# Performance work log

Measured on AMD Instinct MI355X. Metric: run time of the kernel, lower is better.

Reference implementation:

```python
import jax, jax.numpy as jnp
import numpy as np

B, N, D, R, H = 8192, 256, 6, 3, 32


def setup_inputs() -> dict:
    key = jax.random.key(0)
    ks = jax.random.split(key, 8)
    neighbor_states = jax.random.normal(ks[0], (B, N, D), dtype=jnp.float32)
    neighbor_roles = jax.random.randint(ks[1], (B, N), 0, R, dtype=jnp.int32)
    neighbor_mask = jax.random.randint(ks[2], (B, N), 0, 2, dtype=jnp.int32).astype(jnp.bool_)
    trust_weights = jax.random.uniform(ks[3], (B, N), dtype=jnp.float32)
    # per-role MLP params: Linear(D,H) -> ReLU -> Linear(H,1)
    s1 = 1.0 / np.sqrt(D)
    s2 = 1.0 / np.sqrt(H)
    W1 = jax.random.uniform(ks[4], (R, D, H), minval=-s1, maxval=s1, dtype=jnp.float32)
    b1 = jax.random.uniform(ks[5], (R, H), minval=-s1, maxval=s1, dtype=jnp.float32)
    W2 = jax.random.uniform(ks[6], (R, H), minval=-s2, maxval=s2, dtype=jnp.float32)
    b2 = jax.random.uniform(ks[7], (R,), minval=-s2, maxval=s2, dtype=jnp.float32)
    return {
        "neighbor_states": neighbor_states,
        "neighbor_roles": neighbor_roles,
        "neighbor_mask": neighbor_mask,
        "trust_weights": trust_weights,
        "W1": W1, "b1": b1, "W2": W2, "b2": b2,
    }


def reference(neighbor_states, neighbor_roles, neighbor_mask, trust_weights, W1, b1, W2, b2):
    maskf = neighbor_mask.astype(jnp.float32)          # [B, N]
    tw = trust_weights * maskf                          # [B, N]
    # per-role attention scores, vectorized over roles: [B, R, N]
    h = jax.nn.relu(jnp.einsum('bnd,rdh->brnh', neighbor_states, W1) + b1[None, :, None, :])
    scores = jnp.einsum('brnh,rh->brn', h, W2) + b2[None, :, None]
    role_mask = (neighbor_roles[:, None, :] == jnp.arange(R)[None, :, None]).astype(jnp.float32) * maskf[:, None, :]
    scores = scores * role_mask                         # NOTE: multiplicative masking, as in original
    m = scores.max(axis=2, keepdims=True)
    e = jnp.exp(scores - m) * role_mask
    aw = e / (e.sum(axis=2, keepdims=True) + 1e-8)      # [B, R, N]
    w = aw * tw[:, None, :]
    ws = jnp.clip(w.sum(axis=2, keepdims=True), 1e-8)   # [B, R, 1]
    mf = jnp.einsum('brn,bnd->brd', w, neighbor_states) / ws  # [B, R, D]
    return mf.reshape(mf.shape[0], R * D)               # concat roles along last dim
```

## Files before the change

### kernel.cpp

```cpp
#include <hip/hip_runtime.h>
#include <math.h>

#define NBATCH 8192
#define NNEI 256
#define NROLE 3
#define NHID 32
#define NDIM 6
#define SSTRIDE 16

typedef float v2f __attribute__((ext_vector_type(2)));
typedef unsigned long long ull;

__device__ __forceinline__ float mlp_score(const float x0, const float x1,
                                           const float x2, const float x3,
                                           const float x4, const float x5,
                                           const float* __restrict__ w1,
                                           const float* __restrict__ bb,
                                           const float* __restrict__ w2,
                                           const float b2v) {
  const float x[NDIM] = {x0, x1, x2, x3, x4, x5};
  v2f ac0 = {0.f, 0.f}, ac1 = {0.f, 0.f}, ac2 = {0.f, 0.f}, ac3 = {0.f, 0.f};
#pragma unroll
  for (int h = 0; h < NHID; h += 8) {
    v2f a0 = *(const v2f*)(bb + h + 0);
    v2f a1 = *(const v2f*)(bb + h + 2);
    v2f a2 = *(const v2f*)(bb + h + 4);
    v2f a3 = *(const v2f*)(bb + h + 6);
#pragma unroll
    for (int d = 0; d < NDIM; ++d) {
      const float xv = x[d];
      const v2f xv2 = {xv, xv};
      const float* wc = w1 + d * NHID + h;
      a0 += xv2 * (*(const v2f*)(wc + 0));
      a1 += xv2 * (*(const v2f*)(wc + 2));
      a2 += xv2 * (*(const v2f*)(wc + 4));
      a3 += xv2 * (*(const v2f*)(wc + 6));
    }
    a0.x = fmaxf(a0.x, 0.f); a0.y = fmaxf(a0.y, 0.f);
    a1.x = fmaxf(a1.x, 0.f); a1.y = fmaxf(a1.y, 0.f);
    a2.x = fmaxf(a2.x, 0.f); a2.y = fmaxf(a2.y, 0.f);
    a3.x = fmaxf(a3.x, 0.f); a3.y = fmaxf(a3.y, 0.f);
    ac0 += a0 * (*(const v2f*)(w2 + h + 0));
    ac1 += a1 * (*(const v2f*)(w2 + h + 2));
    ac2 += a2 * (*(const v2f*)(w2 + h + 4));
    ac3 += a3 * (*(const v2f*)(w2 + h + 6));
  }
  const v2f st = (ac0 + ac1) + (ac2 + ac3);
  return b2v + st.x + st.y;
}

__global__ __launch_bounds__(256) void hmf_main(
    const float* __restrict__ states,
    const int* __restrict__ roles,
    const int* __restrict__ maskp,
    const float* __restrict__ trust,
    const float* __restrict__ W1,
    const float* __restrict__ b1,
    const float* __restrict__ W2,
    const float* __restrict__ b2g,
    float* __restrict__ out) {
  const int b = blockIdx.x;
  const int tid = threadIdx.x;
  const int wave = tid >> 6;
  const int lane = tid & 63;

  __shared__ float ssort[NNEI * SSTRIDE];
  __shared__ int scnt[12];

  const size_t rowb = (size_t)b * NNEI;
  const int myrole = roles[rowb + tid];
  const int mymask = maskp[rowb + tid];
  const float mytw = trust[rowb + tid];
  const float* sp = states + rowb * NDIM + (size_t)tid * NDIM;
  const float2 sA = *(const float2*)(sp);
  const float2 sB = *(const float2*)(sp + 2);
  const float2 sC = *(const float2*)(sp + 4);
  const bool active = (mymask != 0);

  const ull bal0 = __ballot(active && (myrole == 0));
  const ull bal1 = __ballot(active && (myrole == 1));
  const ull bal2 = __ballot(active && (myrole == 2));
  const int c0 = __popcll(bal0);
  const int c1 = __popcll(bal1);
  const int c2 = __popcll(bal2);
  if (lane < 3) scnt[wave * 3 + lane] = (lane == 0) ? c0 : (lane == 1) ? c1 : c2;

  if (active) {
    const ull mybal = (myrole == 0) ? bal0 : (myrole == 1) ? bal1 : bal2;
    const int rank = __popcll(mybal & ((1ull << lane) - 1ull));
    const int pre = ((myrole >= 1) ? c0 : 0) + ((myrole >= 2) ? c1 : 0);
    const int pos = wave * 64 + pre + rank;
    float* dst = ssort + pos * SSTRIDE;
    *(float4*)dst = make_float4(sA.x, sA.y, sB.x, sB.y);
    *(float2*)(dst + 4) = make_float2(sC.x, sC.y);
    dst[6] = mytw;
  }
  __syncthreads();

  if (wave < 3) {
    const int r = __builtin_amdgcn_readfirstlane(wave);
    int cwv[4], prw[4];
#pragma unroll
    for (int w = 0; w < 4; ++w) {
      const int a0 = scnt[w * 3 + 0];
      const int a1 = scnt[w * 3 + 1];
      const int a2 = scnt[w * 3 + 2];
      const int cv = (r == 0) ? a0 : (r == 1) ? a1 : a2;
      const int pv = ((r >= 1) ? a0 : 0) + ((r >= 2) ? a1 : 0);
      cwv[w] = __builtin_amdgcn_readfirstlane(cv);
      prw[w] = __builtin_amdgcn_readfirstlane(pv);
    }
    const int acc0 = cwv[0];
    const int acc1 = acc0 + cwv[1];
    const int acc2 = acc1 + cwv[2];
    const int cnt = acc2 + cwv[3];

    const float* w1 = W1 + r * (NDIM * NHID);
    const float* bb = b1 + r * NHID;
    const float* w2 = W2 + r * NHID;
    const float b2v = b2g[r];

    float q0, q1, q2, q3, q4, q5, q6, q7;

    if (cnt <= 64) {
      const bool act = lane < cnt;
      const bool s1 = lane >= acc0;
      const bool s2 = lane >= acc1;
      const bool s3 = lane >= acc2;
      int sub = s1 ? acc0 : 0; sub = s2 ? acc1 : sub; sub = s3 ? acc2 : sub;
      int wb = s1 ? 64 : 0;    wb = s2 ? 128 : wb;    wb = s3 ? 192 : wb;
      int pr = s1 ? prw[1] : prw[0]; pr = s2 ? prw[2] : pr; pr = s3 ? prw[3] : pr;
      int pos = wb + pr + (lane - sub);
      pos = (pos > NNEI - 1) ? (NNEI - 1) : pos;
      const float* s = ssort + pos * SSTRIDE;
      float4 v4 = *(const float4*)s;
      float2 v2 = *(const float2*)(s + 4);
      float tw = s[6];
      if (!act) {
        v4 = make_float4(0.f, 0.f, 0.f, 0.f);
        v2 = make_float2(0.f, 0.f);
        tw = 0.f;
      }
      const float sc = mlp_score(v4.x, v4.y, v4.z, v4.w, v2.x, v2.y, w1, bb, w2, b2v);
      const float e = act ? __expf(sc) : 0.f;
      const float et = e * tw;
      q0 = e; q1 = et;
      q2 = et * v4.x; q3 = et * v4.y; q4 = et * v4.z;
      q5 = et * v4.w; q6 = et * v2.x; q7 = et * v2.y;
    } else {
      q0 = q1 = q2 = q3 = q4 = q5 = q6 = q7 = 0.f;
      const int nch = (cnt + 63) >> 6;
      for (int c = 0; c < nch; ++c) {
        const int jj = c * 64 + lane;
        const bool act = jj < cnt;
        const bool s1 = jj >= acc0;
        const bool s2 = jj >= acc1;
        const bool s3 = jj >= acc2;
        int sub = s1 ? acc0 : 0; sub = s2 ? acc1 : sub; sub = s3 ? acc2 : sub;
        int wb = s1 ? 64 : 0;    wb = s2 ? 128 : wb;    wb = s3 ? 192 : wb;
        int pr = s1 ? prw[1] : prw[0]; pr = s2 ? prw[2] : pr; pr = s3 ? prw[3] : pr;
        int pos = wb + pr + (jj - sub);
        pos = (pos > NNEI - 1) ? (NNEI - 1) : pos;
        pos = (pos < 0) ? 0 : pos;
        const float* s = ssort + pos * SSTRIDE;
        float4 v4 = *(const float4*)s;
        float2 v2 = *(const float2*)(s + 4);
        float tw = s[6];
        if (!act) {
          v4 = make_float4(0.f, 0.f, 0.f, 0.f);
          v2 = make_float2(0.f, 0.f);
          tw = 0.f;
        }
        const float sc = mlp_score(v4.x, v4.y, v4.z, v4.w, v2.x, v2.y, w1, bb, w2, b2v);
        const float e = act ? __expf(sc) : 0.f;
        const float et = e * tw;
        q0 += e; q1 += et;
        q2 = fmaf(et, v4.x, q2); q3 = fmaf(et, v4.y, q3);
        q4 = fmaf(et, v4.z, q4); q5 = fmaf(et, v4.w, q5);
        q6 = fmaf(et, v2.x, q6); q7 = fmaf(et, v2.y, q7);
      }
    }

#pragma unroll
    for (int off = 1; off <= 4; off <<= 1) {
      q0 += __shfl_xor(q0, off); q1 += __shfl_xor(q1, off);
      q2 += __shfl_xor(q2, off); q3 += __shfl_xor(q3, off);
      q4 += __shfl_xor(q4, off); q5 += __shfl_xor(q5, off);
      q6 += __shfl_xor(q6, off); q7 += __shfl_xor(q7, off);
    }
    const int g = lane & 7;
    float myq = q0;
    myq = (g == 1) ? q1 : myq;
    myq = (g == 2) ? q2 : myq;
    myq = (g == 3) ? q3 : myq;
    myq = (g == 4) ? q4 : myq;
    myq = (g == 5) ? q5 : myq;
    myq = (g == 6) ? q6 : myq;
    myq = (g == 7) ? q7 : myq;
    myq += __shfl_xor(myq, 8);
    myq += __shfl_xor(myq, 16);
    myq += __shfl_xor(myq, 32);
    const float Se = __shfl(myq, 0);
    const float Set = __shfl(myq, 1);
    const float denom = Se + 1e-8f;
    const float ws = fmaxf(Set / denom, 1e-8f);
    if (lane >= 2 && lane < 8) {
      out[(size_t)b * (NROLE * NDIM) + r * NDIM + (lane - 2)] = (myq / denom) / ws;
    }
  }
}

extern "C" void kernel_launch(void* const* d_in, const int* in_sizes, int n_in,
                              void* d_out, int out_size, void* d_ws, size_t ws_size,
                              hipStream_t stream) {
  const float* states = (const float*)d_in[0];
  const int* roles = (const int*)d_in[1];
  const int* maskp = (const int*)d_in[2];
  const float* trust = (const float*)d_in[3];
  const float* W1 = (const float*)d_in[4];
  const float* b1 = (const float*)d_in[5];
  const float* W2 = (const float*)d_in[6];
  const float* b2 = (const float*)d_in[7];
  float* out = (float*)d_out;

  hmf_main<<<NBATCH, 256, 0, stream>>>(states, roles, maskp, trust, W1, b1, W2, b2, out);
}
```

Baseline: 120.3 us.

## Process four batches per block with register-prefetched next-batch loads

New measurement: 127.7 us. 6.2% more time.

```diff
diff --git a/kernel.cpp b/kernel.cpp
--- a/kernel.cpp
+++ b/kernel.cpp
@@ -7,9 +7,17 @@
 #define NHID 32
 #define NDIM 6
 #define SSTRIDE 16
+#define BPB 4
 
 typedef float v2f __attribute__((ext_vector_type(2)));
 typedef unsigned long long ull;
+
+__device__ __forceinline__ void barrier_lds_only() {
+  __asm__ __volatile__("" ::: "memory");
+  __builtin_amdgcn_s_waitcnt(0xC07F);
+  __builtin_amdgcn_s_barrier();
+  __asm__ __volatile__("" ::: "memory");
+}
 
 __device__ __forceinline__ float mlp_score(const float x0, const float x1,
                                            const float x2, const float x3,
@@ -59,109 +67,98 @@
     const float* __restrict__ W2,
     const float* __restrict__ b2g,
     float* __restrict__ out) {
-  const int b = blockIdx.x;
   const int tid = threadIdx.x;
   const int wave = tid >> 6;
   const int lane = tid & 63;
+  const int b0 = blockIdx.x * BPB;
 
   __shared__ float ssort[NNEI * SSTRIDE];
   __shared__ int scnt[12];
 
-  const size_t rowb = (size_t)b * NNEI;
-  const int myrole = roles[rowb + tid];
-  const int mymask = maskp[rowb + tid];
-  const float mytw = trust[rowb + tid];
+  size_t rowb = (size_t)b0 * NNEI;
+  int n_role = roles[rowb + tid];
+  int n_mask = maskp[rowb + tid];
+  float n_tw = trust[rowb + tid];
   const float* sp = states + rowb * NDIM + (size_t)tid * NDIM;
-  const float2 sA = *(const float2*)(sp);
-  const float2 sB = *(const float2*)(sp + 2);
-  const float2 sC = *(const float2*)(sp + 4);
-  const bool active = (mymask != 0);
-
-  const ull bal0 = __ballot(active && (myrole == 0));
-  const ull bal1 = __ballot(active && (myrole == 1));
-  const ull bal2 = __ballot(active && (myrole == 2));
-  const int c0 = __popcll(bal0);
-  const int c1 = __popcll(bal1);
-  const int c2 = __popcll(bal2);
-  if (lane < 3) scnt[wave * 3 + lane] = (lane == 0) ? c0 : (lane == 1) ? c1 : c2;
-
-  if (active) {
-    const ull mybal = (myrole == 0) ? bal0 : (myrole == 1) ? bal1 : bal2;
-    const int rank = __popcll(mybal & ((1ull << lane) - 1ull));
-    const int pre = ((myrole >= 1) ? c0 : 0) + ((myrole >= 2) ? c1 : 0);
-    const int pos = wave * 64 + pre + rank;
-    float* dst = ssort + pos * SSTRIDE;
-    *(float4*)dst = make_float4(sA.x, sA.y, sB.x, sB.y);
-    *(float2*)(dst + 4) = make_float2(sC.x, sC.y);
-    dst[6] = mytw;
-  }
-  __syncthreads();
-
-  if (wave < 3) {
-    const int r = __builtin_amdgcn_readfirstlane(wave);
-    int cwv[4], prw[4];
-#pragma unroll
-    for (int w = 0; w < 4; ++w) {
-      const int a0 = scnt[w * 3 + 0];
-      const int a1 = scnt[w * 3 + 1];
-      const int a2 = scnt[w * 3 + 2];
-      const int cv = (r == 0) ? a0 : (r == 1) ? a1 : a2;
-      const int pv = ((r >= 1) ? a0 : 0) + ((r >= 2) ? a1 : 0);
-      cwv[w] = __builtin_amdgcn_readfirstlane(cv);
-      prw[w] = __builtin_amdgcn_readfirstlane(pv);
+  float2 n_sA = *(const float2*)(sp);
+  float2 n_sB = *(const float2*)(sp + 2);
+  float2 n_sC = *(const float2*)(sp + 4);
+
+#pragma unroll 1
+  for (int i = 0; i < BPB; ++i) {
+    const int myrole = n_role;
+    const int mymask = n_mask;
+    const float mytw = n_tw;
+    const float2 sA = n_sA;
+    const float2 sB = n_sB;
+    const float2 sC = n_sC;
+
+    const int inext = (i + 1 < BPB) ? (i + 1) : i;
+    rowb = (size_t)(b0 + inext) * NNEI;
+    n_role = roles[rowb + tid];
+    n_mask = maskp[rowb + tid];
+    n_tw = trust[rowb + tid];
+    const float* spn = states + rowb * NDIM + (size_t)tid * NDIM;
+    n_sA = *(const float2*)(spn);
+    n_sB = *(const float2*)(spn + 2);
+    n_sC = *(const float2*)(spn + 4);
+
+    const bool active = (mymask != 0);
+    const ull bal0 = __ballot(active && (myrole == 0));
+    const ull bal1 = __ballot(active && (myrole == 1));
+    const ull bal2 = __ballot(active && (myrole == 2));
+    const int c0 = __popcll(bal0);
+    const int c1 = __popcll(bal1);
+    const int c2 = __popcll(bal2);
+    if (lane < 3) scnt[wave * 3 + lane] = (lane == 0) ? c0 : (lane == 1) ? c1 : c2;
+
+    if (active) {
+      const ull mybal = (myrole == 0) ? bal0 : (myrole == 1) ? bal1 : bal2;
+      const int rank = __popcll(mybal & ((1ull << lane) - 1ull));
+      const int pre = ((myrole >= 1) ? c0 : 0) + ((myrole >= 2) ? c1 : 0);
+      const int pos = wave * 64 + pre + rank;
+      float* dst = ssort + pos * SSTRIDE;
+      *(float4*)dst = make_float4(sA.x, sA.y, sB.x, sB.y);
+      *(float2*)(dst + 4) = make_float2(sC.x, sC.y);
+      dst[6] = mytw;
     }
-    const int acc0 = cwv[0];
-    const int acc1 = acc0 + cwv[1];
-    const int acc2 = acc1 + cwv[2];
-    const int cnt = acc2 + cwv[3];
-
-    const float* w1 = W1 + r * (NDIM * NHID);
-    const float* bb = b1 + r * NHID;
-    const float* w2 = W2 + r * NHID;
-    const float b2v = b2g[r];
-
-    float q0, q1, q2, q3, q4, q5, q6, q7;
-
-    if (cnt <= 64) {
-      const bool act = lane < cnt;
-      const bool s1 = lane >= acc0;
-      const bool s2 = lane >= acc1;
-      const bool s3 = lane >= acc2;
-      int sub = s1 ? acc0 : 0; sub = s2 ? acc1 : sub; sub = s3 ? acc2 : sub;
-      int wb = s1 ? 64 : 0;    wb = s2 ? 128 : wb;    wb = s3 ? 192 : wb;
-      int pr = s1 ? prw[1] : prw[0]; pr = s2 ? prw[2] : pr; pr = s3 ? prw[3] : pr;
-      int pos = wb + pr + (lane - sub);
-      pos = (pos > NNEI - 1) ? (NNEI - 1) : pos;
-      const float* s = ssort + pos * SSTRIDE;
-      float4 v4 = *(const float4*)s;
-      float2 v2 = *(const float2*)(s + 4);
-      float tw = s[6];
-      if (!act) {
-        v4 = make_float4(0.f, 0.f, 0.f, 0.f);
-        v2 = make_float2(0.f, 0.f);
-        tw = 0.f;
-      }
-      const float sc = mlp_score(v4.x, v4.y, v4.z, v4.w, v2.x, v2.y, w1, bb, w2, b2v);
-      const float e = act ? __expf(sc) : 0.f;
-      const float et = e * tw;
-      q0 = e; q1 = et;
-      q2 = et * v4.x; q3 = et * v4.y; q4 = et * v4.z;
-      q5 = et * v4.w; q6 = et * v2.x; q7 = et * v2.y;
-    } else {
-      q0 = q1 = q2 = q3 = q4 = q5 = q6 = q7 = 0.f;
-      const int nch = (cnt + 63) >> 6;
-      for (int c = 0; c < nch; ++c) {
-        const int jj = c * 64 + lane;
-        const bool act = jj < cnt;
-        const bool s1 = jj >= acc0;
-        const bool s2 = jj >= acc1;
-        const bool s3 = jj >= acc2;
+    barrier_lds_only();
+
+    if (wave < 3) {
+      const int r = __builtin_amdgcn_readfirstlane(wave);
+      int cwv[4], prw[4];
+#pragma unroll
+      for (int w = 0; w < 4; ++w) {
+        const int a0 = scnt[w * 3 + 0];
+        const int a1 = scnt[w * 3 + 1];
+        const int a2 = scnt[w * 3 + 2];
+        const int cv = (r == 0) ? a0 : (r == 1) ? a1 : a2;
+        const int pv = ((r >= 1) ? a0 : 0) + ((r >= 2) ? a1 : 0);
+        cwv[w] = __builtin_amdgcn_readfirstlane(cv);
+        prw[w] = __builtin_amdgcn_readfirstlane(pv);
+      }
+      const int acc0 = cwv[0];
+      const int acc1 = acc0 + cwv[1];
+      const int acc2 = acc1 + cwv[2];
+      const int cnt = acc2 + cwv[3];
+
+      const float* w1 = W1 + r * (NDIM * NHID);
+      const float* bb = b1 + r * NHID;
+      const float* w2 = W2 + r * NHID;
+      const float b2v = b2g[r];
+
+      float q0, q1, q2, q3, q4, q5, q6, q7;
+
+      if (cnt <= 64) {
+        const bool act = lane < cnt;
+        const bool s1 = lane >= acc0;
+        const bool s2 = lane >= acc1;
+        const bool s3 = lane >= acc2;
         int sub = s1 ? acc0 : 0; sub = s2 ? acc1 : sub; sub = s3 ? acc2 : sub;
         int wb = s1 ? 64 : 0;    wb = s2 ? 128 : wb;    wb = s3 ? 192 : wb;
         int pr = s1 ? prw[1] : prw[0]; pr = s2 ? prw[2] : pr; pr = s3 ? prw[3] : pr;
-        int pos = wb + pr + (jj - sub);
+        int pos = wb + pr + (lane - sub);
         pos = (pos > NNEI - 1) ? (NNEI - 1) : pos;
-        pos = (pos < 0) ? 0 : pos;
         const float* s = ssort + pos * SSTRIDE;
         float4 v4 = *(const float4*)s;
         float2 v2 = *(const float2*)(s + 4);
@@ -174,39 +171,72 @@
         const float sc = mlp_score(v4.x, v4.y, v4.z, v4.w, v2.x, v2.y, w1, bb, w2, b2v);
         const float e = act ? __expf(sc) : 0.f;
         const float et = e * tw;
-        q0 += e; q1 += et;
-        q2 = fmaf(et, v4.x, q2); q3 = fmaf(et, v4.y, q3);
-        q4 = fmaf(et, v4.z, q4); q5 = fmaf(et, v4.w, q5);
-        q6 = fmaf(et, v2.x, q6); q7 = fmaf(et, v2.y, q7);
+        q0 = e; q1 = et;
+        q2 = et * v4.x; q3 = et * v4.y; q4 = et * v4.z;
+        q5 = et * v4.w; q6 = et * v2.x; q7 = et * v2.y;
+      } else {
+        q0 = q1 = q2 = q3 = q4 = q5 = q6 = q7 = 0.f;
+        const int nch = (cnt + 63) >> 6;
+        for (int c = 0; c < nch; ++c) {
+          const int jj = c * 64 + lane;
+          const bool act = jj < cnt;
+          const bool s1 = jj >= acc0;
+          const bool s2 = jj >= acc1;
+          const bool s3 = jj >= acc2;
+          int sub = s1 ? acc0 : 0; sub = s2 ? acc1 : sub; sub = s3 ? acc2 : sub;
+          int wb = s1 ? 64 : 0;    wb = s2 ? 128 : wb;    wb = s3 ? 192 : wb;
+          int pr = s1 ? prw[1] : prw[0]; pr = s2 ? prw[2] : pr; pr = s3 ? prw[3] : pr;
+          int pos = wb + pr + (jj - sub);
+          pos = (pos > NNEI - 1) ? (NNEI - 1) : pos;
+          pos = (pos < 0) ? 0 : pos;
+          const float* s = ssort + pos * SSTRIDE;
+          float4 v4 = *(const float4*)s;
+          float2 v2 = *(const float2*)(s + 4);
+          float tw = s[6];
+          if (!act) {
+            v4 = make_float4(0.f, 0.f, 0.f, 0.f);
+            v2 = make_float2(0.f, 0.f);
+            tw = 0.f;
+          }
+          const float sc = mlp_score(v4.x, v4.y, v4.z, v4.w, v2.x, v2.y, w1, bb, w2, b2v);
+          const float e = act ? __expf(sc) : 0.f;
+          const float et = e * tw;
+          q0 += e; q1 += et;
+          q2 = fmaf(et, v4.x, q2); q3 = fmaf(et, v4.y, q3);
+          q4 = fmaf(et, v4.z, q4); q5 = fmaf(et, v4.w, q5);
+          q6 = fmaf(et, v2.x, q6); q7 = fmaf(et, v2.y, q7);
+        }
+      }
+
+#pragma unroll
+      for (int off = 1; off <= 4; off <<= 1) {
+        q0 += __shfl_xor(q0, off); q1 += __shfl_xor(q1, off);
+        q2 += __shfl_xor(q2, off); q3 += __shfl_xor(q3, off);
+        q4 += __shfl_xor(q4, off); q5 += __shfl_xor(q5, off);
+        q6 += __shfl_xor(q6, off); q7 += __shfl_xor(q7, off);
+      }
+      const int g = lane & 7;
+      float myq = q0;
+      myq = (g == 1) ? q1 : myq;
+      myq = (g == 2) ? q2 : myq;
+      myq = (g == 3) ? q3 : myq;
+      myq = (g == 4) ? q4 : myq;
+      myq = (g == 5) ? q5 : myq;
+      myq = (g == 6) ? q6 : myq;
+      myq = (g == 7) ? q7 : myq;
+      myq += __shfl_xor(myq, 8);
+      myq += __shfl_xor(myq, 16);
+      myq += __shfl_xor(myq, 32);
+      const float Se = __shfl(myq, 0);
+      const float Set = __shfl(myq, 1);
+      const float denom = Se + 1e-8f;
+      const float ws = fmaxf(Set / denom, 1e-8f);
+      if (lane >= 2 && lane < 8) {
+        out[(size_t)(b0 + i) * (NROLE * NDIM) + r * NDIM + (lane - 2)] =
+            (myq / denom) / ws;
       }
     }
-
-#pragma unroll
-    for (int off = 1; off <= 4; off <<= 1) {
-      q0 += __shfl_xor(q0, off); q1 += __shfl_xor(q1, off);
-      q2 += __shfl_xor(q2, off); q3 += __shfl_xor(q3, off);
-      q4 += __shfl_xor(q4, off); q5 += __shfl_xor(q5, off);
-      q6 += __shfl_xor(q6, off); q7 += __shfl_xor(q7, off);
-    }
-    const int g = lane & 7;
-    float myq = q0;
-    myq = (g == 1) ? q1 : myq;
-    myq = (g == 2) ? q2 : myq;
-    myq = (g == 3) ? q3 : myq;
-    myq = (g == 4) ? q4 : myq;
-    myq = (g == 5) ? q5 : myq;
-    myq = (g == 6) ? q6 : myq;
-    myq = (g == 7) ? q7 : myq;
-    myq += __shfl_xor(myq, 8);
-    myq += __shfl_xor(myq, 16);
-    myq += __shfl_xor(myq, 32);
-    const float Se = __shfl(myq, 0);
-    const float Set = __shfl(myq, 1);
-    const float denom = Se + 1e-8f;
-    const float ws = fmaxf(Set / denom, 1e-8f);
-    if (lane >= 2 && lane < 8) {
-      out[(size_t)b * (NROLE * NDIM) + r * NDIM + (lane - 2)] = (myq / denom) / ws;
-    }
+    barrier_lds_only();
   }
 }
 
@@ -223,5 +253,5 @@
   const float* b2 = (const float*)d_in[7];
   float* out = (float*)d_out;
 
-  hmf_main<<<NBATCH, 256, 0, stream>>>(states, roles, maskp, trust, W1, b1, W2, b2, out);
-}
+  hmf_main<<<NBATCH / BPB, 256, 0, stream>>>(states, roles, maskp, trust, W1, b1, W2, b2, out);
+}
```
